# Kernel tuning notes

Measured on AMD Instinct MI355X. Metric: run time of the kernel, lower is better.

## Reference

```python
import jax, jax.numpy as jnp
import numpy as np

B, L, D, C = 32, 2048, 1024, 1024  # batch, max_length, input_size, context_size


def setup_inputs() -> dict:
    key = jax.random.key(0)
    ks = jax.random.split(key, 4)
    sequence = jax.random.normal(ks[0], (B, L, D), dtype=jnp.float32)
    query = jax.random.normal(ks[1], (B, C), dtype=jnp.float32)
    # lengths in [1, L] so every row has at least one unmasked position
    lengths = jax.random.randint(ks[2], (B,), 1, L + 1, dtype=jnp.int32)
    W_h = jax.random.normal(ks[3], (C, D), dtype=jnp.float32) / np.sqrt(D).astype(np.float32)
    b_h = jnp.zeros((C,), dtype=jnp.float32)
    return {"sequence": sequence, "query": query, "lengths": lengths, "W_h": W_h, "b_h": b_h}


def reference(sequence, query, lengths, W_h, b_h):
    # method='general': energies = (W_h @ sequence + b_h) . query
    h = jnp.einsum('bld,cd->blc', sequence, W_h) + b_h          # [B, L, C]
    energies = jnp.einsum('blc,bc->bl', h, query)                # [B, L]
    # sequence_mask(lengths, L): True where position < length
    mask = jnp.arange(energies.shape[1]) < lengths[:, None]      # [B, L]
    # masked_normalization_inf: fill masked positions with -inf, softmax
    masked = jnp.where(mask, energies, -jnp.inf)
    scores = jax.nn.softmax(masked, axis=-1)                     # [B, L]
    contexts = jnp.einsum('bl,bld->bd', scores, sequence)        # [B, D]
    return contexts, scores
```

## Files before the change

kernel.cpp:

```cpp
#include <hip/hip_runtime.h>
#include <math.h>

#define B_ 32
#define L_ 2048
#define D_ 1024
#define C_ 1024
#define CSPLIT 16
#define WROWS 8
#define BROWS 32
#define NCH (L_ / BROWS)


__global__ __launch_bounds__(256) void k_vpart(const float* __restrict__ q,
                                               const float* __restrict__ W,
                                               float* __restrict__ vpart) {
    int b  = blockIdx.y;
    int cc = blockIdx.x;
    int t  = threadIdx.x;
    const float* qb = q + b * C_;
    float ax = 0.f, ay = 0.f, az = 0.f, aw = 0.f;
    for (int i = 0; i < C_ / CSPLIT; ++i) {
        int c = cc * (C_ / CSPLIT) + i;
        float qv = qb[c];
        float4 w = *reinterpret_cast<const float4*>(W + (size_t)c * D_ + t * 4);
        ax = fmaf(qv, w.x, ax); ay = fmaf(qv, w.y, ay);
        az = fmaf(qv, w.z, az); aw = fmaf(qv, w.w, aw);
    }
    float4 o = {ax, ay, az, aw};
    *reinterpret_cast<float4*>(vpart + ((size_t)cc * B_ + b) * D_ + t * 4) = o;
}

__global__ __launch_bounds__(256) void k_vreduce(const float* __restrict__ vpart,
                                                 float* __restrict__ v,
                                                 const float* __restrict__ q,
                                                 const float* __restrict__ bh,
                                                 float* __restrict__ cb) {
    int b = blockIdx.x, t = threadIdx.x;
    float ax = 0.f, ay = 0.f, az = 0.f, aw = 0.f;
    for (int cc = 0; cc < CSPLIT; ++cc) {
        float4 p = *reinterpret_cast<const float4*>(vpart + ((size_t)cc * B_ + b) * D_ + t * 4);
        ax += p.x; ay += p.y; az += p.z; aw += p.w;
    }
    float4 o = {ax, ay, az, aw};
    *reinterpret_cast<float4*>(v + (size_t)b * D_ + t * 4) = o;

    float s = 0.f;
    for (int c = t; c < C_; c += 256) s += bh[c] * q[b * C_ + c];
    __shared__ float red[256];
    red[t] = s; __syncthreads();
    for (int off = 128; off > 0; off >>= 1) {
        if (t < off) red[t] += red[t + off];
        __syncthreads();
    }
    if (t == 0) cb[b] = red[0];
}

__global__ __launch_bounds__(256) void k_fused(const float* __restrict__ seq,
                                               const float* __restrict__ v,
                                               const float* __restrict__ cb,
                                               const int* __restrict__ lenp,
                                               float* __restrict__ energ,
                                               float* __restrict__ pm,
                                               float* __restrict__ ps,
                                               float* __restrict__ pc) {
    int b  = blockIdx.y;
    int ch = blockIdx.x;
    int len = lenp[b];
    int l0 = ch * BROWS;
    if (l0 >= len) return;
    int wid = threadIdx.x >> 6, lane = threadIdx.x & 63;
    int t = threadIdx.x;
    int lw0 = l0 + wid * WROWS;

    const float* vb = v + (size_t)b * D_;
    float4 v0 = *reinterpret_cast<const float4*>(vb +       lane * 4);
    float4 v1 = *reinterpret_cast<const float4*>(vb + 256 + lane * 4);
    float4 v2 = *reinterpret_cast<const float4*>(vb + 512 + lane * 4);
    float4 v3 = *reinterpret_cast<const float4*>(vb + 768 + lane * 4);
    float cbb = cb[b];

    float m = -INFINITY, s = 0.f;
    float c[16];
    #pragma unroll
    for (int i = 0; i < 16; ++i) c[i] = 0.f;

    __shared__ float e_sm[BROWS];
    __shared__ float lm[4], ls[4];
    __shared__ float lc[4][D_];

    if (lw0 < len) {
        #pragma unroll
        for (int r = 0; r < WROWS; ++r) {
            int l = lw0 + r;
            bool valid = l < len;
            const float* row = seq + ((size_t)b * L_ + l) * D_;
            float4 s0 = *reinterpret_cast<const float4*>(row +       lane * 4);
            float4 s1 = *reinterpret_cast<const float4*>(row + 256 + lane * 4);
            float4 s2 = *reinterpret_cast<const float4*>(row + 512 + lane * 4);
            float4 s3 = *reinterpret_cast<const float4*>(row + 768 + lane * 4);
            float acc = 0.f;
            acc = fmaf(s0.x, v0.x, acc); acc = fmaf(s0.y, v0.y, acc);
            acc = fmaf(s0.z, v0.z, acc); acc = fmaf(s0.w, v0.w, acc);
            acc = fmaf(s1.x, v1.x, acc); acc = fmaf(s1.y, v1.y, acc);
            acc = fmaf(s1.z, v1.z, acc); acc = fmaf(s1.w, v1.w, acc);
            acc = fmaf(s2.x, v2.x, acc); acc = fmaf(s2.y, v2.y, acc);
            acc = fmaf(s2.z, v2.z, acc); acc = fmaf(s2.w, v2.w, acc);
            acc = fmaf(s3.x, v3.x, acc); acc = fmaf(s3.y, v3.y, acc);
            acc = fmaf(s3.z, v3.z, acc); acc = fmaf(s3.w, v3.w, acc);
            #pragma unroll
            for (int off = 32; off; off >>= 1) acc += __shfl_xor(acc, off);
            float e = acc + cbb;
            if (lane == 0) e_sm[wid * WROWS + r] = e;
            float mnew  = valid ? fmaxf(m, e) : m;
            float scale = (m == mnew) ? 1.f : __expf(m - mnew);
            float p     = valid ? __expf(e - mnew) : 0.f;
            s = s * scale + p;
            c[ 0] = fmaf(p, s0.x, c[ 0] * scale); c[ 1] = fmaf(p, s0.y, c[ 1] * scale);
            c[ 2] = fmaf(p, s0.z, c[ 2] * scale); c[ 3] = fmaf(p, s0.w, c[ 3] * scale);
            c[ 4] = fmaf(p, s1.x, c[ 4] * scale); c[ 5] = fmaf(p, s1.y, c[ 5] * scale);
            c[ 6] = fmaf(p, s1.z, c[ 6] * scale); c[ 7] = fmaf(p, s1.w, c[ 7] * scale);
            c[ 8] = fmaf(p, s2.x, c[ 8] * scale); c[ 9] = fmaf(p, s2.y, c[ 9] * scale);
            c[10] = fmaf(p, s2.z, c[10] * scale); c[11] = fmaf(p, s2.w, c[11] * scale);
            c[12] = fmaf(p, s3.x, c[12] * scale); c[13] = fmaf(p, s3.y, c[13] * scale);
            c[14] = fmaf(p, s3.z, c[14] * scale); c[15] = fmaf(p, s3.w, c[15] * scale);
            m = mnew;
        }
    }

    {
        float4 w0 = {c[ 0], c[ 1], c[ 2], c[ 3]};
        float4 w1 = {c[ 4], c[ 5], c[ 6], c[ 7]};
        float4 w2 = {c[ 8], c[ 9], c[10], c[11]};
        float4 w3 = {c[12], c[13], c[14], c[15]};
        *reinterpret_cast<float4*>(&lc[wid][      lane * 4]) = w0;
        *reinterpret_cast<float4*>(&lc[wid][256 + lane * 4]) = w1;
        *reinterpret_cast<float4*>(&lc[wid][512 + lane * 4]) = w2;
        *reinterpret_cast<float4*>(&lc[wid][768 + lane * 4]) = w3;
        if (lane == 0) { lm[wid] = m; ls[wid] = s; }
    }
    __syncthreads();

    if (t < BROWS) energ[(size_t)b * L_ + l0 + t] = e_sm[t];

    float mb = fmaxf(fmaxf(lm[0], lm[1]), fmaxf(lm[2], lm[3]));
    float w0 = (lm[0] == mb) ? 1.f : __expf(lm[0] - mb);
    float w1 = (lm[1] == mb) ? 1.f : __expf(lm[1] - mb);
    float w2 = (lm[2] == mb) ? 1.f : __expf(lm[2] - mb);
    float w3 = (lm[3] == mb) ? 1.f : __expf(lm[3] - mb);
    float sb = w0 * ls[0] + w1 * ls[1] + w2 * ls[2] + w3 * ls[3];

    float4 a0 = *reinterpret_cast<const float4*>(&lc[0][t * 4]);
    float4 a1 = *reinterpret_cast<const float4*>(&lc[1][t * 4]);
    float4 a2 = *reinterpret_cast<const float4*>(&lc[2][t * 4]);
    float4 a3 = *reinterpret_cast<const float4*>(&lc[3][t * 4]);
    float4 o;
    o.x = w0 * a0.x + w1 * a1.x + w2 * a2.x + w3 * a3.x;
    o.y = w0 * a0.y + w1 * a1.y + w2 * a2.y + w3 * a3.y;
    o.z = w0 * a0.z + w1 * a1.z + w2 * a2.z + w3 * a3.z;
    o.w = w0 * a0.w + w1 * a1.w + w2 * a2.w + w3 * a3.w;

    size_t pidx = (size_t)b * NCH + ch;
    if (t == 0) { pm[pidx] = mb; ps[pidx] = sb; }
    *reinterpret_cast<float4*>(pc + pidx * D_ + t * 4) = o;
}

__global__ __launch_bounds__(256) void k_final(const float* __restrict__ pm,
                                               const float* __restrict__ ps,
                                               const float* __restrict__ pc,
                                               const float* __restrict__ energ,
                                               const int* __restrict__ lenp,
                                               float* __restrict__ ctx,
                                               float* __restrict__ scores) {
    int b = blockIdx.x, t = threadIdx.x;
    int len = lenp[b];
    int nch = (len + BROWS - 1) / BROWS;
    __shared__ float wgt[NCH];
    __shared__ float Msh, Ssh;
    if (t < 64) {
        float mi = (t < nch) ? pm[(size_t)b * NCH + t] : -INFINITY;
        float si = (t < nch) ? ps[(size_t)b * NCH + t] : 0.f;
        float M = mi;
        #pragma unroll
        for (int off = 32; off; off >>= 1) M = fmaxf(M, __shfl_xor(M, off));
        float ew = (t < nch) ? __expf(mi - M) : 0.f;
        float S  = ew * si;
        #pragma unroll
        for (int off = 32; off; off >>= 1) S += __shfl_xor(S, off);
        if (t < nch) wgt[t] = ew / S;
        if (t == 0) { Msh = M; Ssh = S; }
    }
    __syncthreads();
    float M = Msh;
    float invS = 1.f / Ssh;

    float4 o = {0.f, 0.f, 0.f, 0.f};
    for (int ch = 0; ch < nch; ++ch) {
        float w = wgt[ch];
        float4 p = *reinterpret_cast<const float4*>(pc + ((size_t)b * NCH + ch) * D_ + t * 4);
        o.x = fmaf(w, p.x, o.x); o.y = fmaf(w, p.y, o.y);
        o.z = fmaf(w, p.z, o.z); o.w = fmaf(w, p.w, o.w);
    }
    *reinterpret_cast<float4*>(ctx + (size_t)b * D_ + t * 4) = o;

    #pragma unroll
    for (int i = 0; i < L_ / 256; ++i) {
        int l = i * 256 + t;
        float e = energ[(size_t)b * L_ + l];
        scores[(size_t)b * L_ + l] = (l < len) ? __expf(e - M) * invS : 0.f;
    }
}

extern "C" void kernel_launch(void* const* d_in, const int* in_sizes, int n_in,
                              void* d_out, int out_size, void* d_ws, size_t ws_size,
                              hipStream_t stream) {
    const float* seq     = (const float*)d_in[0];
    const float* query   = (const float*)d_in[1];
    const int*   lengths = (const int*)  d_in[2];
    const float* W_h     = (const float*)d_in[3];
    const float* b_h     = (const float*)d_in[4];

    float* out    = (float*)d_out;
    float* ctx    = out;
    float* scores = out + B_ * D_;

    float* ws    = (float*)d_ws;
    float* v     = ws;
    float* cb    = ws + 32768;
    float* energ = ws + 32800;
    float* vpart = ws + 98336;
    float* pm    = ws + 622624;
    float* ps    = ws + 624672;
    float* pc    = ws + 626720;

    k_vpart  <<<dim3(CSPLIT, B_), 256, 0, stream>>>(query, W_h, vpart);
    k_vreduce<<<B_, 256, 0, stream>>>(vpart, v, query, b_h, cb);
    k_fused  <<<dim3(NCH, B_), 256, 0, stream>>>(seq, v, cb, lengths, energ, pm, ps, pc);
    k_final  <<<B_, 256, 0, stream>>>(pm, ps, pc, energ, lengths, ctx, scores);
}
```

Baseline: 49.07 us.

## Tile query-weight product across batches and parallelize reduce and final kernels

Rewrites the q·W projection so each block stages a 64-column query slice for all batches in shared memory and reads each W tile once, instead of every batch re-reading all of W. The reduce and final kernels gain a second grid dimension to split work over D and L, raising block count from 32 to 128 and 256. The final kernel redundantly recomputes the chunk softmax statistics in every slice block, and the ctx accumulation now uses scalar loads with half the threads.

```diff
diff --git a/kernel.cpp b/kernel.cpp
--- a/kernel.cpp
+++ b/kernel.cpp
@@ -5,7 +5,6 @@
 #define L_ 2048
 #define D_ 1024
 #define C_ 1024
-#define CSPLIT 16
 #define WROWS 8
 #define BROWS 32
 #define NCH (L_ / BROWS)
@@ -14,20 +13,33 @@
 __global__ __launch_bounds__(256) void k_vpart(const float* __restrict__ q,
                                                const float* __restrict__ W,
                                                float* __restrict__ vpart) {
-    int b  = blockIdx.y;
-    int cc = blockIdx.x;
+    int cc = blockIdx.x, dc = blockIdx.y;
     int t  = threadIdx.x;
-    const float* qb = q + b * C_;
-    float ax = 0.f, ay = 0.f, az = 0.f, aw = 0.f;
-    for (int i = 0; i < C_ / CSPLIT; ++i) {
-        int c = cc * (C_ / CSPLIT) + i;
-        float qv = qb[c];
-        float4 w = *reinterpret_cast<const float4*>(W + (size_t)c * D_ + t * 4);
-        ax = fmaf(qv, w.x, ax); ay = fmaf(qv, w.y, ay);
-        az = fmaf(qv, w.z, az); aw = fmaf(qv, w.w, aw);
-    }
-    float4 o = {ax, ay, az, aw};
-    *reinterpret_cast<float4*>(vpart + ((size_t)cc * B_ + b) * D_ + t * 4) = o;
+    __shared__ float qs[B_][65];
+    #pragma unroll
+    for (int i = 0; i < 8; ++i) {
+        int idx = t + i * 256;
+        int b = idx >> 6, cl = idx & 63;
+        qs[b][cl] = q[b * C_ + cc * 64 + cl];
+    }
+    __syncthreads();
+
+    int dl4 = t & 15;
+    int bg  = t >> 4;
+    float4 a0 = {0,0,0,0}, a1 = {0,0,0,0};
+    const float4* W4 = reinterpret_cast<const float4*>(W);
+    for (int c = 0; c < 64; ++c) {
+        float4 w = W4[(size_t)(cc * 64 + c) * (D_ / 4) + dc * 16 + dl4];
+        float q0 = qs[bg * 2 + 0][c];
+        float q1 = qs[bg * 2 + 1][c];
+        a0.x = fmaf(q0, w.x, a0.x); a0.y = fmaf(q0, w.y, a0.y);
+        a0.z = fmaf(q0, w.z, a0.z); a0.w = fmaf(q0, w.w, a0.w);
+        a1.x = fmaf(q1, w.x, a1.x); a1.y = fmaf(q1, w.y, a1.y);
+        a1.z = fmaf(q1, w.z, a1.z); a1.w = fmaf(q1, w.w, a1.w);
+    }
+    size_t base = ((size_t)cc * B_ + bg * 2) * D_ + dc * 64 + dl4 * 4;
+    *reinterpret_cast<float4*>(vpart + base)       = a0;
+    *reinterpret_cast<float4*>(vpart + base + D_)  = a1;
 }
 
 __global__ __launch_bounds__(256) void k_vreduce(const float* __restrict__ vpart,
@@ -35,24 +47,25 @@
                                                  const float* __restrict__ q,
                                                  const float* __restrict__ bh,
                                                  float* __restrict__ cb) {
-    int b = blockIdx.x, t = threadIdx.x;
-    float ax = 0.f, ay = 0.f, az = 0.f, aw = 0.f;
-    for (int cc = 0; cc < CSPLIT; ++cc) {
-        float4 p = *reinterpret_cast<const float4*>(vpart + ((size_t)cc * B_ + b) * D_ + t * 4);
-        ax += p.x; ay += p.y; az += p.z; aw += p.w;
-    }
-    float4 o = {ax, ay, az, aw};
-    *reinterpret_cast<float4*>(v + (size_t)b * D_ + t * 4) = o;
-
-    float s = 0.f;
-    for (int c = t; c < C_; c += 256) s += bh[c] * q[b * C_ + c];
-    __shared__ float red[256];
-    red[t] = s; __syncthreads();
-    for (int off = 128; off > 0; off >>= 1) {
-        if (t < off) red[t] += red[t + off];
-        __syncthreads();
-    }
-    if (t == 0) cb[b] = red[0];
+    int b = blockIdx.x, dq = blockIdx.y, t = threadIdx.x;
+    int d = dq * 256 + t;
+    float a = 0.f;
+    #pragma unroll
+    for (int cc = 0; cc < 16; ++cc)
+        a += vpart[((size_t)cc * B_ + b) * D_ + d];
+    v[(size_t)b * D_ + d] = a;
+
+    if (dq == 0) {
+        float s = 0.f;
+        for (int c = t; c < C_; c += 256) s += bh[c] * q[b * C_ + c];
+        __shared__ float red[256];
+        red[t] = s; __syncthreads();
+        for (int off = 128; off > 0; off >>= 1) {
+            if (t < off) red[t] += red[t + off];
+            __syncthreads();
+        }
+        if (t == 0) cb[b] = red[0];
+    }
 }
 
 __global__ __launch_bounds__(256) void k_fused(const float* __restrict__ seq,
@@ -171,7 +184,7 @@
                                                const int* __restrict__ lenp,
                                                float* __restrict__ ctx,
                                                float* __restrict__ scores) {
-    int b = blockIdx.x, t = threadIdx.x;
+    int b = blockIdx.x, sl = blockIdx.y, t = threadIdx.x;
     int len = lenp[b];
     int nch = (len + BROWS - 1) / BROWS;
     __shared__ float wgt[NCH];
@@ -193,21 +206,17 @@
     float M = Msh;
     float invS = 1.f / Ssh;
 
-    float4 o = {0.f, 0.f, 0.f, 0.f};
-    for (int ch = 0; ch < nch; ++ch) {
-        float w = wgt[ch];
-        float4 p = *reinterpret_cast<const float4*>(pc + ((size_t)b * NCH + ch) * D_ + t * 4);
-        o.x = fmaf(w, p.x, o.x); o.y = fmaf(w, p.y, o.y);
-        o.z = fmaf(w, p.z, o.z); o.w = fmaf(w, p.w, o.w);
-    }
-    *reinterpret_cast<float4*>(ctx + (size_t)b * D_ + t * 4) = o;
-
-    #pragma unroll
-    for (int i = 0; i < L_ / 256; ++i) {
-        int l = i * 256 + t;
-        float e = energ[(size_t)b * L_ + l];
-        scores[(size_t)b * L_ + l] = (l < len) ? __expf(e - M) * invS : 0.f;
-    }
+    if (t < 128) {
+        int d = sl * 128 + t;
+        float o = 0.f;
+        for (int ch = 0; ch < nch; ++ch)
+            o = fmaf(wgt[ch], pc[((size_t)b * NCH + ch) * D_ + d], o);
+        ctx[(size_t)b * D_ + d] = o;
+    }
+
+    int l = sl * 256 + t;
+    float e = energ[(size_t)b * L_ + l];
+    scores[(size_t)b * L_ + l] = (l < len) ? __expf(e - M) * invS : 0.f;
 }
 
 extern "C" void kernel_launch(void* const* d_in, const int* in_sizes, int n_in,
@@ -232,8 +241,8 @@
     float* ps    = ws + 624672;
     float* pc    = ws + 626720;
 
-    k_vpart  <<<dim3(CSPLIT, B_), 256, 0, stream>>>(query, W_h, vpart);
-    k_vreduce<<<B_, 256, 0, stream>>>(vpart, v, query, b_h, cb);
+    k_vpart  <<<dim3(16, 16), 256, 0, stream>>>(query, W_h, vpart);
+    k_vreduce<<<dim3(B_, 4), 256, 0, stream>>>(vpart, v, query, b_h, cb);
     k_fused  <<<dim3(NCH, B_), 256, 0, stream>>>(seq, v, cb, lengths, energ, pm, ps, pc);
-    k_final  <<<B_, 256, 0, stream>>>(pm, ps, pc, energ, lengths, ctx, scores);
-}
+    k_final  <<<dim3(B_, 8), 256, 0, stream>>>(pm, ps, pc, energ, lengths, ctx, scores);
+}
```

After: 46.86 us. 4.5% less time.
